# Kernel tuning notes

Hardware: AMD Instinct MI355X
Metric: run time of the kernel (lower is better)

Reference implementation:

```python
import jax, jax.numpy as jnp
import numpy as np

K_NODES = 512  # per-expert capacity (k_nodes init arg)


def setup_inputs() -> dict:
    key = jax.random.key(0)
    k1, k2, k3, k4 = jax.random.split(key, 4)
    B_T, D, E = 16384, 512, 64
    x = jax.random.normal(k1, (B_T, D, 2), jnp.float32)
    # gate: orthogonal_(gain=0.1) ~ small-scale dense matrix
    gate_weights = jax.random.normal(k2, (2 * D, E), jnp.float32) * (0.1 / np.sqrt(2 * D))
    # ComplexKaimingInitializer: |N(0,1)|/sqrt(fan_in) magnitude, uniform phase
    mag = jnp.abs(jax.random.normal(k3, (E, D, D), jnp.float32)) / np.sqrt(D)
    phase = jax.random.uniform(k4, (E, D, D), jnp.float32, minval=0.0, maxval=2.0 * np.pi)
    experts_w = jnp.stack([mag * jnp.cos(phase), mag * jnp.sin(phase)], axis=-1)  # [E,D,D,2]
    act_bias = jnp.zeros((D,), jnp.float32)
    return {"x": x, "gate_weights": gate_weights, "experts_w": experts_w, "act_bias": act_bias}


def reference(x, gate_weights, experts_w, act_bias):
    # x: [B_T, D, 2] interleaved-real tokens
    B_T, D, _ = x.shape
    E = gate_weights.shape[1]
    k = min(B_T, K_NODES)

    # --- expert-choice routing: each expert picks its top-k tokens ---
    scores = jnp.nan_to_num(x.reshape(B_T, 2 * D) @ gate_weights)  # [B_T, E]
    topk_scores, topk_idx = jax.lax.top_k(scores.T, k)             # [E, k] each

    # --- gather tokens per expert (row-major [E, k] order, as in forward()) ---
    flat_gather = topk_idx.reshape(-1)                  # [E*k]
    xb = x[flat_gather].reshape(E, k, D, 2)             # [E, k, D, 2]
    xr, xi = xb[..., 0], xb[..., 1]
    wr, wi = experts_w[..., 0], experts_w[..., 1]

    # --- grouped complex GEMM as 4 real batched matmuls ---
    yr = jnp.einsum('ekd,edf->ekf', xr, wr) - jnp.einsum('ekd,edf->ekf', xi, wi)
    yi = jnp.einsum('ekd,edf->ekf', xr, wi) + jnp.einsum('ekd,edf->ekf', xi, wr)
    y = jnp.nan_to_num(jnp.stack([yr, yi], axis=-1))    # [E, k, D, 2]

    # weight by routing scores, then scatter-add combine
    y_weighted = (y * topk_scores[..., None, None]).reshape(E * k, D, 2)
    # NOTE: original code scatters with topk_indices.T.reshape(-1) (column-major
    # w.r.t. the [E,k] gather order). Reproduced faithfully.
    flat_scatter = topk_idx.T.reshape(-1)               # [E*k]
    out = jnp.zeros((B_T, D, 2), jnp.float32).at[flat_scatter].add(y_weighted)
    counts = jnp.zeros((B_T,), jnp.float32).at[flat_scatter].add(1.0)
    agg = out / jnp.maximum(counts, 1.0)[:, None, None]

    # ComplexGELU: exact (erf) GELU on real/imag parts with shared bias
    res = jax.nn.gelu(agg + act_bias[:, None], approximate=False)  # [B_T, D, 2]
    return res
```

## Files before the change

kernel.cpp:

```cpp
#include <hip/hip_runtime.h>
#include <stdint.h>
#include <math.h>

typedef uint32_t u32;
typedef uint64_t u64;
typedef unsigned short u16;

#define B_T    16384
#define DD     512
#define NE     64
#define KCAP   512
#define TWO_D  1024

typedef __attribute__((ext_vector_type(8))) short bf16x8;
typedef __attribute__((ext_vector_type(4))) float f32x4;
typedef __attribute__((ext_vector_type(4))) u32 u32x4;

static __device__ __forceinline__ u32 mono_of(float s) {
  u32 b = __float_as_uint(s);
  return (b & 0x80000000u) ? ~b : (b | 0x80000000u);
}
static __device__ __forceinline__ float score_from_mono(u32 m) {
  u32 b = (m & 0x80000000u) ? (m ^ 0x80000000u) : ~m;
  return __uint_as_float(b);
}
static __device__ __forceinline__ u16 f2bf(float f) {
  u32 b = __float_as_uint(f);
  b += 0x7FFFu + ((b >> 16) & 1u);
  return (u16)(b >> 16);
}
static __device__ __forceinline__ u32 f2bf2(float lo, float hi) {
  return (u32)f2bf(lo) | ((u32)f2bf(hi) << 16);
}
static __device__ __forceinline__ float bf2f(u32 u) {
  return __uint_as_float(u << 16);
}
static __device__ __forceinline__ u32 cvtpk(float lo, float hi) {
  u32 r;
  asm("v_cvt_pk_bf16_f32 %0, %1, %2" : "=v"(r) : "v"(lo), "v"(hi));
  return r;
}
static __device__ __forceinline__ void gload_lds16(const u16* g, u16* l) {
  __builtin_amdgcn_global_load_lds(
      (const __attribute__((address_space(1))) u32*)(g),
      (__attribute__((address_space(3))) u32*)(l), 16, 0, 0);
}
static __device__ __forceinline__ bf16x8 negbf8(bf16x8 v) {
  u32x4 u;
  u32x4 s = *reinterpret_cast<u32x4*>(&v);
  u[0] = s[0] ^ 0x80008000u;
  u[1] = s[1] ^ 0x80008000u;
  u[2] = s[2] ^ 0x80008000u;
  u[3] = s[3] ^ 0x80008000u;
  return *reinterpret_cast<bf16x8*>(&u);
}

__global__ __launch_bounds__(256) void k0_xconv(const float* __restrict__ x,
                                                u16* __restrict__ xrb,
                                                u16* __restrict__ xib) {
  int idx = blockIdx.x * 256 + threadIdx.x;
  float4 v = reinterpret_cast<const float4*>(x)[idx];
  reinterpret_cast<u32*>(xrb)[idx] = f2bf2(v.x, v.z);
  reinterpret_cast<u32*>(xib)[idx] = f2bf2(v.y, v.w);
}

__global__ __launch_bounds__(256) void k1_gate(const float* __restrict__ x,
                                               const float* __restrict__ gw,
                                               float* __restrict__ scoresT) {
  __shared__ __align__(16) float xs[128][64];
  __shared__ __align__(16) float gs[128][64];
  const int tb  = blockIdx.x * 64;
  const int tid = threadIdx.x;
  const int tx = tid & 15, ty = tid >> 4;

  float accC[4][4];
  float accT[4][4];
#pragma unroll
  for (int i = 0; i < 4; ++i)
#pragma unroll
    for (int j = 0; j < 4; ++j) { accC[i][j] = 0.f; accT[i][j] = 0.f; }

  for (int c = 0; c < 8; ++c) {
    const int k0 = c * 128;
    {
      const int t = tid & 63, ks = (tid >> 6) * 32;
      const float* src = x + (size_t)(tb + t) * TWO_D + k0 + ks;
#pragma unroll
      for (int i = 0; i < 8; ++i) {
        float4 v = reinterpret_cast<const float4*>(src)[i];
        xs[ks + i * 4 + 0][t] = v.x;
        xs[ks + i * 4 + 1][t] = v.y;
        xs[ks + i * 4 + 2][t] = v.z;
        xs[ks + i * 4 + 3][t] = v.w;
      }
      const float4* gsrc = reinterpret_cast<const float4*>(gw + (size_t)k0 * 64);
      float4* gdst = reinterpret_cast<float4*>(&gs[0][0]);
#pragma unroll
      for (int i = 0; i < 8; ++i) gdst[tid + i * 256] = gsrc[tid + i * 256];
    }
    __syncthreads();
    for (int k = 0; k < 128; ++k) {
      float4 a4 = *reinterpret_cast<float4*>(&xs[k][tx * 4]);
      float4 b4 = *reinterpret_cast<float4*>(&gs[k][ty * 4]);
      float av[4] = {a4.x, a4.y, a4.z, a4.w};
      float bv[4] = {b4.x, b4.y, b4.z, b4.w};
#pragma unroll
      for (int i = 0; i < 4; ++i)
#pragma unroll
        for (int j = 0; j < 4; ++j) accC[i][j] = fmaf(bv[i], av[j], accC[i][j]);
    }
    __syncthreads();
    if (c == 3 || c == 7) {
#pragma unroll
      for (int i = 0; i < 4; ++i)
#pragma unroll
        for (int j = 0; j < 4; ++j) {
          accT[i][j] = accT[i][j] + accC[i][j];
          accC[i][j] = 0.f;
        }
    }
  }
#pragma unroll
  for (int i = 0; i < 4; ++i) {
    float4 v = make_float4(accT[i][0], accT[i][1], accT[i][2], accT[i][3]);
    *reinterpret_cast<float4*>(&scoresT[(size_t)(ty * 4 + i) * B_T + tb + tx * 4]) = v;
  }
}

__global__ __launch_bounds__(1024) void k2_topk(const float* __restrict__ scoresT,
                                                int* __restrict__ topk_idx,
                                                float* __restrict__ topk_scr,
                                                int* __restrict__ counts,
                                                int* __restrict__ entries) {
  const int e = blockIdx.x, tid = threadIdx.x;
  const float* row = scoresT + (size_t)e * B_T;
  __shared__ u32 keys[B_T];
  __shared__ u32 hist[256];
  __shared__ u32 s_prefix, s_r;
  __shared__ u32 cnt_gt, cnt_eq;
  __shared__ u64 skey[512];
  __shared__ u32 tie[512];

#pragma unroll
  for (int i = 0; i < 4; ++i) {
    int v4 = i * 1024 + tid;
    float4 v = reinterpret_cast<const float4*>(row)[v4];
    keys[v4 * 4 + 0] = mono_of(v.x);
    keys[v4 * 4 + 1] = mono_of(v.y);
    keys[v4 * 4 + 2] = mono_of(v.z);
    keys[v4 * 4 + 3] = mono_of(v.w);
  }
  if (tid == 0) { s_prefix = 0; s_r = KCAP; cnt_gt = 0; cnt_eq = 0; }
  u32 prefmask = 0;
  __syncthreads();

  for (int pass = 0; pass < 4; ++pass) {
    const int shift = 24 - 8 * pass;
    if (tid < 256) hist[tid] = 0;
    __syncthreads();
    const u32 prefix = s_prefix;
    for (int t = tid; t < B_T; t += 1024) {
      u32 m = keys[t];
      if ((m & prefmask) == prefix) atomicAdd(&hist[(m >> shift) & 0xFFu], 1u);
    }
    __syncthreads();
    if (tid == 0) {
      u32 r = s_r, cum = 0;
      int sel = 0;
      for (int b = 255; b >= 0; --b) {
        if (cum + hist[b] >= r) { sel = b; s_r = r - cum; break; }
        cum += hist[b];
      }
      s_prefix = prefix | ((u32)sel << shift);
    }
    prefmask |= (0xFFu << shift);
    __syncthreads();
  }

  const u32 kmono = s_prefix;
  const u32 rneed = s_r;

  for (int t = tid; t < B_T; t += 1024) {
    u32 m = keys[t];
    if (m > kmono) {
      u32 p = atomicAdd(&cnt_gt, 1u);
      if (p < 512) skey[p] = ((u64)(~m) << 32) | (u32)t;
    } else if (m == kmono) {
      u32 p = atomicAdd(&cnt_eq, 1u);
      if (p < 512) tie[p] = (u32)t;
    }
  }
  __syncthreads();

  const u32 ngt = cnt_gt;
  const u32 ne = cnt_eq < 512u ? cnt_eq : 512u;
  if (tid < ne) {
    u32 my = tie[tid];
    u32 rank = 0;
    for (u32 j = 0; j < ne; ++j) rank += (tie[j] < my) ? 1u : 0u;
    if (rank < rneed) skey[ngt + rank] = ((u64)(~kmono) << 32) | my;
  }
  __syncthreads();

  if (tid < 512) {
    u64 my = skey[tid];
    u32 rank = 0;
    for (int j = 0; j < 512; ++j) rank += (skey[j] < my) ? 1u : 0u;
    u32 idx = (u32)my;
    u32 m = ~((u32)(my >> 32));
    topk_idx[e * KCAP + rank] = (int)idx;
    topk_scr[e * KCAP + rank] = score_from_mono(m);
    int pos = atomicAdd(&counts[idx], 1);
    entries[idx * 64 + pos] = (int)(rank * 64 + e);
  }
}

__global__ __launch_bounds__(256) void k3_wtrans(const float* __restrict__ w,
                                                 u16* __restrict__ wrT,
                                                 u16* __restrict__ wiT) {
  __shared__ float2 tr[32][33];
  const int bid = blockIdx.x;
  const int e = bid >> 8, tile = bid & 255;
  const int d0 = (tile >> 4) * 32, f0 = (tile & 15) * 32;
  const int tid = threadIdx.x;
  const int fl2 = tid & 15, dl0 = tid >> 4;
  const float* base = w + ((size_t)e * 512 + d0) * 1024 + (size_t)f0 * 2;
#pragma unroll
  for (int it = 0; it < 2; ++it) {
    int dl = dl0 + it * 16;
    float4 v = *reinterpret_cast<const float4*>(base + (size_t)dl * 1024 + fl2 * 4);
    tr[dl][fl2 * 2]     = make_float2(v.x, v.y);
    tr[dl][fl2 * 2 + 1] = make_float2(v.z, v.w);
  }
  __syncthreads();
  const int d2 = (tid & 15) * 2, fl0 = tid >> 4;
#pragma unroll
  for (int it = 0; it < 2; ++it) {
    int f = fl0 + it * 16;
    float2 a = tr[d2][f], b = tr[d2 + 1][f];
    size_t off = ((size_t)e * 512 + f0 + f) * 512 + d0 + d2;
    *reinterpret_cast<u32*>(&wrT[off]) = f2bf2(a.x, b.x);
    *reinterpret_cast<u32*>(&wiT[off]) = f2bf2(a.y, b.y);
  }
}

template <int PRECONV>
__global__ __launch_bounds__(256, 2) void k4_gemm(
    const float* __restrict__ x, const u16* __restrict__ xrb,
    const u16* __restrict__ xib, const int* __restrict__ topk_idx,
    const float* __restrict__ topk_scr, const u16* __restrict__ wrT,
    const u16* __restrict__ wiT, u16* __restrict__ yrw, u16* __restrict__ yiw) {
  const int bid = blockIdx.x;
  const int xcd = bid & 7, q = bid >> 3, t = q & 15, g = q >> 4;
  const int e = g * 8 + xcd;
  const int mb = t & 3, fb = t >> 2;
  const int m0 = mb * 128, f0 = fb * 128;

  __shared__ __align__(16) u16 Ar[4096];
  __shared__ __align__(16) u16 Ai[4096];
  __shared__ __align__(16) u16 Bu[4096];
  __shared__ __align__(16) u16 Bv[4096];
  __shared__ int tok[128];
  __shared__ float scr[128];

  const int tid = threadIdx.x;
  if (tid < 128) {
    tok[tid] = topk_idx[e * KCAP + m0 + tid];
    scr[tid] = topk_scr[e * KCAP + m0 + tid];
  }
  __syncthreads();

  const int r0  = tid & 127;
  const int ka0 = (tid >> 7) * 8;
  const int ka1 = ka0 + 16;
  const size_t brow = ((size_t)e * 512 + f0 + r0) * 512;
  const int wv = tid >> 6, ln = tid & 63;
  const int d0 = wv * 512;
  const int d1 = 2048 + wv * 512;

  const int mytok = tok[r0];
  const size_t arow_bf = (size_t)mytok * 512;
  const int row = tid >> 1, half = tid & 1;
  const float* arow_f = x + (size_t)tok[row] * TWO_D + half * 32;

  const int mbase = (wv >> 1) * 64, nbase = (wv & 1) * 64;
  const int frow = ln & 15, fq = ln >> 4;
  const int ra = fq * 1024 + (mbase + frow) * 8;
  const int rb = fq * 1024 + (nbase + frow) * 8;

  f32x4 accR[4][4] = {};
  f32x4 accI[4][4] = {};

  for (int step = 0; step < 16; ++step) {
    const int k0 = step * 32;
    gload_lds16(wrT + brow + k0 + ka0, Bu + d0);
    gload_lds16(wrT + brow + k0 + ka1, Bu + d1);
    gload_lds16(wiT + brow + k0 + ka0, Bv + d0);
    gload_lds16(wiT + brow + k0 + ka1, Bv + d1);
    if (PRECONV) {
      gload_lds16(xrb + arow_bf + k0 + ka0, Ar + d0);
      gload_lds16(xrb + arow_bf + k0 + ka1, Ar + d1);
      gload_lds16(xib + arow_bf + k0 + ka0, Ai + d0);
      gload_lds16(xib + arow_bf + k0 + ka1, Ai + d1);
    } else {
      const float4* ap = reinterpret_cast<const float4*>(arow_f + (size_t)k0 * 2);
      u32 xr[8], xi[8];
#pragma unroll
      for (int i = 0; i < 8; ++i) {
        float4 v = ap[i];
        xr[i] = cvtpk(v.x, v.z);
        xi[i] = cvtpk(v.y, v.w);
      }
      uint4 wa, wb;
      wa.x = xr[0]; wa.y = xr[1]; wa.z = xr[2]; wa.w = xr[3];
      wb.x = xr[4]; wb.y = xr[5]; wb.z = xr[6]; wb.w = xr[7];
      *reinterpret_cast<uint4*>(&Ar[(2 * half) * 1024 + row * 8]) = wa;
      *reinterpret_cast<uint4*>(&Ar[(2 * half + 1) * 1024 + row * 8]) = wb;
      wa.x = xi[0]; wa.y = xi[1]; wa.z = xi[2]; wa.w = xi[3];
      wb.x = xi[4]; wb.y = xi[5]; wb.z = xi[6]; wb.w = xi[7];
      *reinterpret_cast<uint4*>(&Ai[(2 * half) * 1024 + row * 8]) = wa;
      *reinterpret_cast<uint4*>(&Ai[(2 * half + 1) * 1024 + row * 8]) = wb;
    }
    __syncthreads();

    bf16x8 ar[4], ai[4], bu[4], bv[4];
#pragma unroll
    for (int m = 0; m < 4; ++m) {
      ar[m] = *reinterpret_cast<const bf16x8*>(&Ar[ra + m * 128]);
      ai[m] = *reinterpret_cast<const bf16x8*>(&Ai[ra + m * 128]);
    }
#pragma unroll
    for (int n = 0; n < 4; ++n) {
      bu[n] = *reinterpret_cast<const bf16x8*>(&Bu[rb + n * 128]);
      bv[n] = *reinterpret_cast<const bf16x8*>(&Bv[rb + n * 128]);
    }
#pragma unroll
    for (int m = 0; m < 4; ++m)
#pragma unroll
      for (int n = 0; n < 4; ++n) {
        bf16x8 bw = negbf8(bv[n]);
        accR[m][n] = __builtin_amdgcn_mfma_f32_16x16x32_bf16(ar[m], bu[n], accR[m][n], 0, 0, 0);
        accR[m][n] = __builtin_amdgcn_mfma_f32_16x16x32_bf16(ai[m], bw,    accR[m][n], 0, 0, 0);
        accI[m][n] = __builtin_amdgcn_mfma_f32_16x16x32_bf16(ar[m], bv[n], accI[m][n], 0, 0, 0);
        accI[m][n] = __builtin_amdgcn_mfma_f32_16x16x32_bf16(ai[m], bu[n], accI[m][n], 0, 0, 0);
      }
    __syncthreads();
  }

  const int rr = fq * 4;
#pragma unroll
  for (int m = 0; m < 4; ++m) {
#pragma unroll
    for (int r = 0; r < 4; ++r) {
      const int jl = mbase + m * 16 + rr + r;
      const float ww = scr[jl];
      const size_t ybase = ((size_t)e * KCAP + m0 + jl) * DD;
#pragma unroll
      for (int n = 0; n < 4; ++n) {
        const int fg = f0 + nbase + n * 16 + frow;
        yrw[ybase + fg] = f2bf(accR[m][n][r] * ww);
        yiw[ybase + fg] = f2bf(accI[m][n][r] * ww);
      }
    }
  }
}

#define GELU(z) (0.5f * (z) * (1.0f + erff((z)*0.70710678118654752440f)))
__global__ __launch_bounds__(256) void k5_gather(
    const u16* __restrict__ yrw, const u16* __restrict__ yiw,
    const int* __restrict__ counts, const int* __restrict__ entries,
    const float* __restrict__ bias, float* __restrict__ out) {
  const int t = blockIdx.x;
  const int tid = threadIdx.x;
  const int c = counts[t];
  const float inv = 1.0f / (float)(c > 0 ? c : 1);
  const int f0 = tid * 2;
  float sr0 = 0.f, sr1 = 0.f, si0 = 0.f, si1 = 0.f;
  for (int i = 0; i < c; ++i) {
    int srcrow = entries[t * 64 + i];
    size_t off = (size_t)srcrow * DD + f0;
    u32 pr = *reinterpret_cast<const u32*>(yrw + off);
    u32 pi = *reinterpret_cast<const u32*>(yiw + off);
    sr0 += bf2f(pr & 0xFFFFu); sr1 += bf2f(pr >> 16);
    si0 += bf2f(pi & 0xFFFFu); si1 += bf2f(pi >> 16);
  }
  const float b0 = bias[f0], b1 = bias[f0 + 1];
  float v0 = sr0 * inv + b0;
  float v1 = si0 * inv + b0;
  float v2 = sr1 * inv + b1;
  float v3 = si1 * inv + b1;
  float4 o = make_float4(GELU(v0), GELU(v1), GELU(v2), GELU(v3));
  *reinterpret_cast<float4*>(&out[(size_t)t * TWO_D + f0 * 2]) = o;
}

extern "C" void kernel_launch(void* const* d_in, const int* in_sizes, int n_in,
                              void* d_out, int out_size, void* d_ws, size_t ws_size,
                              hipStream_t stream) {
  const float* x    = (const float*)d_in[0];
  const float* gw   = (const float*)d_in[1];
  const float* w    = (const float*)d_in[2];
  const float* bias = (const float*)d_in[3];
  float* out = (float*)d_out;

  char* ws = (char*)d_ws;
  u16*   yrw     = (u16*)(ws);
  float* scoresT = (float*)(ws);
  u16*   yiw     = (u16*)(ws + 33554432);
  int*   tidx    = (int*)(ws + 67108864);
  float* tscr    = (float*)(ws + 67239936);
  int*   counts  = (int*)(ws + 67371008);
  int*   entries = (int*)(ws + 67436544);
  u16*   wrT     = (u16*)(ws + 71630848);
  u16*   wiT     = (u16*)(ws + 105185280);
  u16*   xrb     = (u16*)(ws + 138739712);
  u16*   xib     = (u16*)(ws + 155516928);

  const bool preconv = ws_size >= 172294144ull;

  hipMemsetAsync(counts, 0, B_T * sizeof(int), stream);
  k1_gate<<<B_T / 64, 256, 0, stream>>>(x, gw, scoresT);
  k2_topk<<<NE, 1024, 0, stream>>>(scoresT, tidx, tscr, counts, entries);
  k3_wtrans<<<NE * 256, 256, 0, stream>>>(w, wrT, wiT);
  if (preconv) {
    k0_xconv<<<16384, 256, 0, stream>>>(x, xrb, xib);
    k4_gemm<1><<<1024, 256, 0, stream>>>(x, xrb, xib, tidx, tscr, wrT, wiT, yrw, yiw);
  } else {
    k4_gemm<0><<<1024, 256, 0, stream>>>(x, nullptr, nullptr, tidx, tscr, wrT, wiT, yrw, yiw);
  }
  k5_gather<<<B_T, 256, 0, stream>>>(yrw, yiw, counts, entries, bias, out);
}
```

Baseline: 287.2 us.

## Double-buffer LDS in preconverted expert GEMM and halve gate tile size

Splits the expert GEMM into a preconverted-input variant that double-buffers its A and B LDS tiles, so the global-to-LDS loads for the next K step are issued while MFMAs run on the current one. It also halves the gate-score kernel's token tile to 32, doubling its block count to improve occupancy. The GEMM doubles LDS use to about 64KB per block, which may cut the two blocks per CU it targets, and needs only one barrier per step. The gate kernel now does less work per thread, with lower register reuse.

```diff
diff --git a/kernel.cpp b/kernel.cpp
--- a/kernel.cpp
+++ b/kernel.cpp
@@ -67,26 +67,26 @@
 __global__ __launch_bounds__(256) void k1_gate(const float* __restrict__ x,
                                                const float* __restrict__ gw,
                                                float* __restrict__ scoresT) {
-  __shared__ __align__(16) float xs[128][64];
+  __shared__ __align__(16) float xs[128][32];
   __shared__ __align__(16) float gs[128][64];
-  const int tb  = blockIdx.x * 64;
+  const int tb  = blockIdx.x * 32;
   const int tid = threadIdx.x;
-  const int tx = tid & 15, ty = tid >> 4;
-
-  float accC[4][4];
-  float accT[4][4];
-#pragma unroll
-  for (int i = 0; i < 4; ++i)
+  const int tx = tid & 7, ty = tid >> 3;
+
+  float accC[2][4];
+  float accT[2][4];
+#pragma unroll
+  for (int i = 0; i < 2; ++i)
 #pragma unroll
     for (int j = 0; j < 4; ++j) { accC[i][j] = 0.f; accT[i][j] = 0.f; }
 
   for (int c = 0; c < 8; ++c) {
     const int k0 = c * 128;
     {
-      const int t = tid & 63, ks = (tid >> 6) * 32;
+      const int t = tid & 31, ks = (tid >> 5) * 16;
       const float* src = x + (size_t)(tb + t) * TWO_D + k0 + ks;
 #pragma unroll
-      for (int i = 0; i < 8; ++i) {
+      for (int i = 0; i < 4; ++i) {
         float4 v = reinterpret_cast<const float4*>(src)[i];
         xs[ks + i * 4 + 0][t] = v.x;
         xs[ks + i * 4 + 1][t] = v.y;
@@ -101,18 +101,18 @@
     __syncthreads();
     for (int k = 0; k < 128; ++k) {
       float4 a4 = *reinterpret_cast<float4*>(&xs[k][tx * 4]);
-      float4 b4 = *reinterpret_cast<float4*>(&gs[k][ty * 4]);
+      float2 b2 = *reinterpret_cast<float2*>(&gs[k][ty * 2]);
       float av[4] = {a4.x, a4.y, a4.z, a4.w};
-      float bv[4] = {b4.x, b4.y, b4.z, b4.w};
-#pragma unroll
-      for (int i = 0; i < 4; ++i)
+      float bv[2] = {b2.x, b2.y};
+#pragma unroll
+      for (int i = 0; i < 2; ++i)
 #pragma unroll
         for (int j = 0; j < 4; ++j) accC[i][j] = fmaf(bv[i], av[j], accC[i][j]);
     }
     __syncthreads();
     if (c == 3 || c == 7) {
 #pragma unroll
-      for (int i = 0; i < 4; ++i)
+      for (int i = 0; i < 2; ++i)
 #pragma unroll
         for (int j = 0; j < 4; ++j) {
           accT[i][j] = accT[i][j] + accC[i][j];
@@ -121,9 +121,9 @@
     }
   }
 #pragma unroll
-  for (int i = 0; i < 4; ++i) {
+  for (int i = 0; i < 2; ++i) {
     float4 v = make_float4(accT[i][0], accT[i][1], accT[i][2], accT[i][3]);
-    *reinterpret_cast<float4*>(&scoresT[(size_t)(ty * 4 + i) * B_T + tb + tx * 4]) = v;
+    *reinterpret_cast<float4*>(&scoresT[(size_t)(ty * 2 + i) * B_T + tb + tx * 4]) = v;
   }
 }
 
@@ -244,10 +244,112 @@
   }
 }
 
-template <int PRECONV>
-__global__ __launch_bounds__(256, 2) void k4_gemm(
-    const float* __restrict__ x, const u16* __restrict__ xrb,
-    const u16* __restrict__ xib, const int* __restrict__ topk_idx,
+__global__ __launch_bounds__(256, 2) void k4_pre(
+    const u16* __restrict__ xrb, const u16* __restrict__ xib,
+    const int* __restrict__ topk_idx, const float* __restrict__ topk_scr,
+    const u16* __restrict__ wrT, const u16* __restrict__ wiT,
+    u16* __restrict__ yrw, u16* __restrict__ yiw) {
+  const int bid = blockIdx.x;
+  const int xcd = bid & 7, q = bid >> 3, t = q & 15, g = q >> 4;
+  const int e = g * 8 + xcd;
+  const int mb = t & 3, fb = t >> 2;
+  const int m0 = mb * 128, f0 = fb * 128;
+
+  __shared__ __align__(16) u16 Ar[2][4096];
+  __shared__ __align__(16) u16 Ai[2][4096];
+  __shared__ __align__(16) u16 Bu[2][4096];
+  __shared__ __align__(16) u16 Bv[2][4096];
+  __shared__ int tok[128];
+  __shared__ float scr[128];
+
+  const int tid = threadIdx.x;
+  if (tid < 128) {
+    tok[tid] = topk_idx[e * KCAP + m0 + tid];
+    scr[tid] = topk_scr[e * KCAP + m0 + tid];
+  }
+  __syncthreads();
+
+  const int r0  = tid & 127;
+  const int ka0 = (tid >> 7) * 8;
+  const int ka1 = ka0 + 16;
+  const size_t brow = ((size_t)e * 512 + f0 + r0) * 512;
+  const size_t arow = (size_t)tok[r0] * 512;
+  const int wv = tid >> 6, ln = tid & 63;
+  const int d0 = wv * 512;
+  const int d1 = 2048 + wv * 512;
+
+  const int mbase = (wv >> 1) * 64, nbase = (wv & 1) * 64;
+  const int frow = ln & 15, fq = ln >> 4;
+  const int ra = fq * 1024 + (mbase + frow) * 8;
+  const int rb = fq * 1024 + (nbase + frow) * 8;
+
+  f32x4 accR[4][4] = {};
+  f32x4 accI[4][4] = {};
+
+#define STAGE(b, kk)                                         \
+  do {                                                       \
+    gload_lds16(wrT + brow + (kk) + ka0, Bu[b] + d0);        \
+    gload_lds16(wrT + brow + (kk) + ka1, Bu[b] + d1);        \
+    gload_lds16(wiT + brow + (kk) + ka0, Bv[b] + d0);        \
+    gload_lds16(wiT + brow + (kk) + ka1, Bv[b] + d1);        \
+    gload_lds16(xrb + arow + (kk) + ka0, Ar[b] + d0);        \
+    gload_lds16(xrb + arow + (kk) + ka1, Ar[b] + d1);        \
+    gload_lds16(xib + arow + (kk) + ka0, Ai[b] + d0);        \
+    gload_lds16(xib + arow + (kk) + ka1, Ai[b] + d1);        \
+  } while (0)
+
+  STAGE(0, 0);
+  __syncthreads();
+
+  for (int s = 0; s < 16; ++s) {
+    const int b = s & 1;
+    if (s < 15) STAGE(b ^ 1, (s + 1) * 32);
+
+    bf16x8 ar[4], ai[4], bu[4], bv[4];
+#pragma unroll
+    for (int m = 0; m < 4; ++m) {
+      ar[m] = *reinterpret_cast<const bf16x8*>(&Ar[b][ra + m * 128]);
+      ai[m] = *reinterpret_cast<const bf16x8*>(&Ai[b][ra + m * 128]);
+    }
+#pragma unroll
+    for (int n = 0; n < 4; ++n) {
+      bu[n] = *reinterpret_cast<const bf16x8*>(&Bu[b][rb + n * 128]);
+      bv[n] = *reinterpret_cast<const bf16x8*>(&Bv[b][rb + n * 128]);
+    }
+#pragma unroll
+    for (int m = 0; m < 4; ++m)
+#pragma unroll
+      for (int n = 0; n < 4; ++n) {
+        bf16x8 bw = negbf8(bv[n]);
+        accR[m][n] = __builtin_amdgcn_mfma_f32_16x16x32_bf16(ar[m], bu[n], accR[m][n], 0, 0, 0);
+        accR[m][n] = __builtin_amdgcn_mfma_f32_16x16x32_bf16(ai[m], bw,    accR[m][n], 0, 0, 0);
+        accI[m][n] = __builtin_amdgcn_mfma_f32_16x16x32_bf16(ar[m], bv[n], accI[m][n], 0, 0, 0);
+        accI[m][n] = __builtin_amdgcn_mfma_f32_16x16x32_bf16(ai[m], bu[n], accI[m][n], 0, 0, 0);
+      }
+    __syncthreads();
+  }
+#undef STAGE
+
+  const int rr = fq * 4;
+#pragma unroll
+  for (int m = 0; m < 4; ++m) {
+#pragma unroll
+    for (int r = 0; r < 4; ++r) {
+      const int jl = mbase + m * 16 + rr + r;
+      const float ww = scr[jl];
+      const size_t ybase = ((size_t)e * KCAP + m0 + jl) * DD;
+#pragma unroll
+      for (int n = 0; n < 4; ++n) {
+        const int fg = f0 + nbase + n * 16 + frow;
+        yrw[ybase + fg] = f2bf(accR[m][n][r] * ww);
+        yiw[ybase + fg] = f2bf(accI[m][n][r] * ww);
+      }
+    }
+  }
+}
+
+__global__ __launch_bounds__(256, 2) void k4_fb(
+    const float* __restrict__ x, const int* __restrict__ topk_idx,
     const float* __restrict__ topk_scr, const u16* __restrict__ wrT,
     const u16* __restrict__ wiT, u16* __restrict__ yrw, u16* __restrict__ yiw) {
   const int bid = blockIdx.x;
@@ -278,8 +380,6 @@
   const int d0 = wv * 512;
   const int d1 = 2048 + wv * 512;
 
-  const int mytok = tok[r0];
-  const size_t arow_bf = (size_t)mytok * 512;
   const int row = tid >> 1, half = tid & 1;
   const float* arow_f = x + (size_t)tok[row] * TWO_D + half * 32;
 
@@ -297,12 +397,7 @@
     gload_lds16(wrT + brow + k0 + ka1, Bu + d1);
     gload_lds16(wiT + brow + k0 + ka0, Bv + d0);
     gload_lds16(wiT + brow + k0 + ka1, Bv + d1);
-    if (PRECONV) {
-      gload_lds16(xrb + arow_bf + k0 + ka0, Ar + d0);
-      gload_lds16(xrb + arow_bf + k0 + ka1, Ar + d1);
-      gload_lds16(xib + arow_bf + k0 + ka0, Ai + d0);
-      gload_lds16(xib + arow_bf + k0 + ka1, Ai + d1);
-    } else {
+    {
       const float4* ap = reinterpret_cast<const float4*>(arow_f + (size_t)k0 * 2);
       u32 xr[8], xi[8];
 #pragma unroll
@@ -418,14 +513,14 @@
   const bool preconv = ws_size >= 172294144ull;
 
   hipMemsetAsync(counts, 0, B_T * sizeof(int), stream);
-  k1_gate<<<B_T / 64, 256, 0, stream>>>(x, gw, scoresT);
+  k1_gate<<<B_T / 32, 256, 0, stream>>>(x, gw, scoresT);
   k2_topk<<<NE, 1024, 0, stream>>>(scoresT, tidx, tscr, counts, entries);
   k3_wtrans<<<NE * 256, 256, 0, stream>>>(w, wrT, wiT);
   if (preconv) {
     k0_xconv<<<16384, 256, 0, stream>>>(x, xrb, xib);
-    k4_gemm<1><<<1024, 256, 0, stream>>>(x, xrb, xib, tidx, tscr, wrT, wiT, yrw, yiw);
+    k4_pre<<<1024, 256, 0, stream>>>(xrb, xib, tidx, tscr, wrT, wiT, yrw, yiw);
   } else {
-    k4_gemm<0><<<1024, 256, 0, stream>>>(x, nullptr, nullptr, tidx, tscr, wrT, wiT, yrw, yiw);
+    k4_fb<<<1024, 256, 0, stream>>>(x, tidx, tscr, wrT, wiT, yrw, yiw);
   }
   k5_gather<<<B_T, 256, 0, stream>>>(yrw, yiw, counts, entries, bias, out);
 }
```

Result: no change. 290.7 us (+1.2%).
